# Kernel tuning notes

Hardware: AMD Instinct MI355X
Metric: run time of the kernel (lower is better)

Reference implementation:

```python
import jax, jax.numpy as jnp
import numpy as np

N, E, IN, OUT, R, B = 50000, 800000, 16, 16, 90, 30


def setup_inputs() -> dict:
    key = jax.random.key(0)
    ks = jax.random.split(key, 9)
    h = jax.random.normal(ks[0], (N, IN), dtype=jnp.float32)
    he = jax.random.normal(ks[1], (E, IN), dtype=jnp.float32)
    Ws = jax.random.normal(ks[2], (OUT, IN), dtype=jnp.float32) * 0.1      # shared_weight.weight
    Wa = jax.random.normal(ks[3], (1, 3 * OUT), dtype=jnp.float32) * 0.1   # attn_fc.weight
    weight = jax.random.normal(ks[4], (B, IN, OUT), dtype=jnp.float32) * 0.1  # basis weights
    w_comp = jax.random.normal(ks[5], (R, B), dtype=jnp.float32) * 0.1        # basis coefficients
    src = jax.random.randint(ks[6], (E,), 0, N)
    dst = jax.random.randint(ks[7], (E,), 0, N)
    rel_type = jax.random.randint(ks[8], (E,), 0, R)
    return {"h": h, "he": he, "Ws": Ws, "Wa": Wa, "weight": weight,
            "w_comp": w_comp, "src": src, "dst": dst, "rel_type": rel_type}


def reference(h, he, Ws, Wa, weight, w_comp, src, dst, rel_type):
    n_nodes, in_dim = h.shape
    num_bases, _, out_dim = weight.shape
    num_rels = w_comp.shape[0]

    # Basis decomposition, replicating the original's reshape semantics exactly:
    # view [B,in,out] -> [in,B,out], matmul with w_comp [R,B] -> [in,R,out], view -> [R,in,out]
    V = weight.reshape(in_dim, num_bases, out_dim)
    W_rel = jnp.matmul(w_comp, V).reshape(num_rels, in_dim, out_dim)  # [R,in,out]

    # edge_attention: GAT-like score from concat(z_src, z_edge, z_dst)
    h_src = h[src]                      # [E,in]
    z_src = h_src @ Ws.T                # [E,out]
    z_dst = h[dst] @ Ws.T               # [E,out]
    z_e = he @ Ws.T                     # [E,out]
    e = jnp.concatenate([z_src, z_e, z_dst], axis=1) @ Wa.T  # [E,1] (no leaky_relu / no softmax in original)

    # message: per-edge relation-specific bmm, scaled by attention score
    msg = jnp.einsum('ei,eio->eo', h_src, W_rel[rel_type]) * e  # [E,out]

    # reduce: scatter-sum into destination nodes (bias=None, activation=None)
    h_out = jax.ops.segment_sum(msg, dst, num_segments=n_nodes)  # [N,out]
    return h_out
```

## Files before the change

kernel.cpp:

```cpp
#include <hip/hip_runtime.h>

#define N_NODES 50000
#define N_EDGES 800000
#define IN_DIM 16
#define OUT_DIM 16
#define N_RELS 90
#define N_BASES 30

#define CAP 64
#define LDS_STRIDE 260

#define PREP_BLOCKS 91
#define DOTS_BLOCKS 196
#define ZERO_BLOCKS 196
#define HZ_BLOCKS 782

#define ROUTE_BLOCKS 3125
#define RNODES_PER_BLK 64
#define REDUCE_BLOCKS 782

__device__ __forceinline__ float4 shfl_xor4(float4 v, int m) {
    float4 r;
    r.x = __shfl_xor(v.x, m); r.y = __shfl_xor(v.y, m);
    r.z = __shfl_xor(v.z, m); r.w = __shfl_xor(v.w, m);
    return r;
}

__global__ __launch_bounds__(256) void setup_kernel(
    const float* __restrict__ Ws,
    const float* __restrict__ Wa,
    const float* __restrict__ weight,
    const float* __restrict__ w_comp,
    const float* __restrict__ h,
    float* __restrict__ Wrel,
    float* __restrict__ avec,
    float2* __restrict__ s13,
    int* __restrict__ cnt,
    float* __restrict__ hout)
{
    int b = blockIdx.x;
    if (b < PREP_BLOCKS) {
        int f = b * 256 + threadIdx.x;
        if (f < N_RELS * IN_DIM * OUT_DIM) {
            int a   = f / (N_RELS * OUT_DIM);
            int rem = f % (N_RELS * OUT_DIM);
            int r   = rem / OUT_DIM;
            int o   = rem % OUT_DIM;
            float acc = 0.f;
            #pragma unroll
            for (int bb = 0; bb < N_BASES; ++bb)
                acc += w_comp[r * N_BASES + bb] * weight[a * (N_BASES * OUT_DIM) + bb * OUT_DIM + o];
            Wrel[f] = acc;
        } else if (f < N_RELS * IN_DIM * OUT_DIM + 48) {
            int g = f - N_RELS * IN_DIM * OUT_DIM;
            int k = g / IN_DIM;
            int i = g % IN_DIM;
            float acc = 0.f;
            #pragma unroll
            for (int o = 0; o < OUT_DIM; ++o)
                acc += Wa[k * OUT_DIM + o] * Ws[o * IN_DIM + i];
            avec[g] = acc;
        }
    } else if (b < PREP_BLOCKS + DOTS_BLOCKS) {
        __shared__ float la[48];
        if (threadIdx.x < 48) {
            int k = threadIdx.x / IN_DIM;
            int i = threadIdx.x % IN_DIM;
            float acc = 0.f;
            #pragma unroll
            for (int o = 0; o < OUT_DIM; ++o)
                acc += Wa[k * OUT_DIM + o] * Ws[o * IN_DIM + i];
            la[threadIdx.x] = acc;
        }
        __syncthreads();
        int n = (b - PREP_BLOCKS) * 256 + threadIdx.x;
        if (n >= N_NODES) return;
        const float4* p = (const float4*)(h + (size_t)n * IN_DIM);
        float d1 = 0.f, d3 = 0.f;
        #pragma unroll
        for (int i = 0; i < 4; ++i) {
            float4 v = p[i];
            d1 += v.x * la[4*i+0] + v.y * la[4*i+1] + v.z * la[4*i+2] + v.w * la[4*i+3];
            d3 += v.x * la[32+4*i+0] + v.y * la[32+4*i+1] + v.z * la[32+4*i+2] + v.w * la[32+4*i+3];
        }
        s13[n] = make_float2(d1, d3);
    } else if (b < PREP_BLOCKS + DOTS_BLOCKS + ZERO_BLOCKS) {
        int n = (b - PREP_BLOCKS - DOTS_BLOCKS) * 256 + threadIdx.x;
        if (n < N_NODES) cnt[n] = 0;
    } else {
        int idx = (b - PREP_BLOCKS - DOTS_BLOCKS - ZERO_BLOCKS) * 256 + threadIdx.x;
        if (idx < N_NODES * OUT_DIM / 4) {
            float4 z = {0.f, 0.f, 0.f, 0.f};
            ((float4*)hout)[idx] = z;
        }
    }
}

__global__ __launch_bounds__(256) void route_kernel(
    const float* __restrict__ h,
    const float* __restrict__ he,
    const int* __restrict__ src,
    const int* __restrict__ dst,
    const int* __restrict__ rel,
    const float* __restrict__ Wrel,
    const float* __restrict__ avec,
    const float2* __restrict__ s13,
    int* __restrict__ cnt,
    uint2* __restrict__ bucket,
    float* __restrict__ hout)
{
    int e = blockIdx.x * 256 + threadIdx.x;
    if (e >= N_EDGES) return;
    int s = src[e], d = dst[e], r = rel[e];

    const float4* hep = (const float4*)(he + (size_t)e * IN_DIM);
    const float4* ap  = (const float4*)(avec + 16);
    float pd = 0.f;
    #pragma unroll
    for (int i = 0; i < 4; ++i) {
        float4 v = hep[i];
        float4 a = ap[i];
        pd += v.x * a.x + v.y * a.y + v.z * a.z + v.w * a.w;
    }

    int slot = atomicAdd(&cnt[d], 1);
    if (slot < CAP) {
        uint2 ent;
        ent.x = ((unsigned)r << 16) | (unsigned)s;
        ent.y = __float_as_uint(pd);
        bucket[(size_t)d * CAP + slot] = ent;
    } else {
        float2 ss = s13[s];
        float2 sd = s13[d];
        float score = ss.x + sd.y + pd;
        float hs[16];
        const float4* hp = (const float4*)(h + (size_t)s * IN_DIM);
        #pragma unroll
        for (int i = 0; i < 4; ++i) {
            float4 v = hp[i];
            hs[4*i+0] = v.x; hs[4*i+1] = v.y; hs[4*i+2] = v.z; hs[4*i+3] = v.w;
        }
        const float* W = Wrel + (size_t)r * 256;
        float* outp = hout + (size_t)d * OUT_DIM;
        #pragma unroll
        for (int o = 0; o < OUT_DIM; ++o) {
            float acc = 0.f;
            #pragma unroll
            for (int i = 0; i < IN_DIM; ++i) acc += hs[i] * W[i * OUT_DIM + o];
            atomicAdd(outp + o, acc * score);
        }
    }
}

__global__ __launch_bounds__(1024) void reduce_bmm_kernel(
    const float* __restrict__ h,
    const float* __restrict__ Wrel,
    const float2* __restrict__ s13,
    const uint2* __restrict__ bucket,
    const int* __restrict__ cnt,
    float* __restrict__ hout)
{
    extern __shared__ float lw[];
    for (int j = threadIdx.x; j < N_RELS * 64; j += 1024) {
        int r = j >> 6;
        int w = j & 63;
        float4 v = ((const float4*)Wrel)[r * 64 + w];
        *(float4*)(lw + r * LDS_STRIDE + w * 4) = v;
    }
    __syncthreads();

    int n = blockIdx.x * RNODES_PER_BLK + (threadIdx.x >> 4);
    int l = threadIdx.x & 15;
    int q = l & 3;
    int p = l >> 2;
    if (n >= N_NODES) return;

    int deg = cnt[n];
    int m = deg > CAP ? CAP : deg;
    const uint2* ep = bucket + (size_t)n * CAP;
    float s3n = s13[n].y;
    float4 acc = {0.f, 0.f, 0.f, 0.f};

    for (int j0 = 0; j0 < m; j0 += 8) {
        uint2 ent[2];
        float4 hq[2];
        float s1v[2];
        bool val[2];

        #pragma unroll
        for (int k = 0; k < 2; ++k) {
            int j = j0 + p * 2 + k;
            val[k] = (j < m);
            ent[k] = ep[val[k] ? j : 0];
        }

        #pragma unroll
        for (int k = 0; k < 2; ++k) {
            int sidx = ent[k].x & 0xFFFF;
            hq[k]  = *(const float4*)(h + (size_t)sidx * IN_DIM + q * 4);
            s1v[k] = s13[sidx].x;
        }

        #pragma unroll
        for (int k = 0; k < 2; ++k) {
            if (!val[k]) continue;
            int r = ent[k].x >> 16;
            float score = s1v[k] + s3n + __uint_as_float(ent[k].y);

            float4 o1 = shfl_xor4(hq[k], 1);
            float4 o2 = shfl_xor4(hq[k], 2);
            float4 o3 = shfl_xor4(o1, 2);
            bool q0 = (q == 0), q1 = (q == 1), q2 = (q == 2);
            float4 row0 = q0 ? hq[k] : q1 ? o1 : q2 ? o2 : o3;
            float4 row1 = q0 ? o1 : q1 ? hq[k] : q2 ? o3 : o2;
            float4 row2 = q0 ? o2 : q1 ? o3 : q2 ? hq[k] : o1;
            float4 row3 = q0 ? o3 : q1 ? o2 : q2 ? o1 : hq[k];
            float hs[16] = {row0.x,row0.y,row0.z,row0.w, row1.x,row1.y,row1.z,row1.w,
                            row2.x,row2.y,row2.z,row2.w, row3.x,row3.y,row3.z,row3.w};

            const float* wb = lw + (size_t)r * LDS_STRIDE + q * 4;
            float4 a = {0.f, 0.f, 0.f, 0.f};
            #pragma unroll
            for (int i = 0; i < 16; ++i) {
                float4 w = *(const float4*)(wb + i * 16);
                float hv = hs[i];
                a.x += hv * w.x; a.y += hv * w.y; a.z += hv * w.z; a.w += hv * w.w;
            }
            acc.x += score * a.x; acc.y += score * a.y;
            acc.z += score * a.z; acc.w += score * a.w;
        }
    }

    acc.x += __shfl_xor(acc.x, 4); acc.y += __shfl_xor(acc.y, 4);
    acc.z += __shfl_xor(acc.z, 4); acc.w += __shfl_xor(acc.w, 4);
    acc.x += __shfl_xor(acc.x, 8); acc.y += __shfl_xor(acc.y, 8);
    acc.z += __shfl_xor(acc.z, 8); acc.w += __shfl_xor(acc.w, 8);

    if (p == 0) {
        float* outp = hout + (size_t)n * OUT_DIM + q * 4;
        if (deg <= CAP) {
            *(float4*)outp = acc;
        } else {
            atomicAdd(outp + 0, acc.x);
            atomicAdd(outp + 1, acc.y);
            atomicAdd(outp + 2, acc.z);
            atomicAdd(outp + 3, acc.w);
        }
    }
}

__global__ __launch_bounds__(256) void prep_kernel(
    const float* __restrict__ Ws, const float* __restrict__ Wa,
    const float* __restrict__ weight, const float* __restrict__ w_comp,
    float* __restrict__ Wrel, float* __restrict__ avec)
{
    int f = blockIdx.x * blockDim.x + threadIdx.x;
    if (f < N_RELS * IN_DIM * OUT_DIM) {
        int a   = f / (N_RELS * OUT_DIM);
        int rem = f % (N_RELS * OUT_DIM);
        int r   = rem / OUT_DIM;
        int o   = rem % OUT_DIM;
        float acc = 0.f;
        #pragma unroll
        for (int b = 0; b < N_BASES; ++b)
            acc += w_comp[r * N_BASES + b] * weight[a * (N_BASES * OUT_DIM) + b * OUT_DIM + o];
        Wrel[f] = acc;
    } else if (f < N_RELS * IN_DIM * OUT_DIM + 48) {
        int g = f - N_RELS * IN_DIM * OUT_DIM;
        int k = g / IN_DIM;
        int i = g % IN_DIM;
        float acc = 0.f;
        #pragma unroll
        for (int o = 0; o < OUT_DIM; ++o)
            acc += Wa[k * OUT_DIM + o] * Ws[o * IN_DIM + i];
        avec[g] = acc;
    }
}

__global__ __launch_bounds__(256) void edge_atomic_kernel(
    const float* __restrict__ h,
    const float* __restrict__ he,
    const int* __restrict__ src,
    const int* __restrict__ dst,
    const int* __restrict__ rel,
    const float* __restrict__ Wrel,
    const float* __restrict__ avec,
    float* __restrict__ hout)
{
    int e = blockIdx.x * blockDim.x + threadIdx.x;
    if (e >= N_EDGES) return;
    int s = src[e], d = dst[e], r = rel[e];
    float hs[IN_DIM];
    const float4* p = (const float4*)(h + (size_t)s * IN_DIM);
    #pragma unroll
    for (int i = 0; i < 4; ++i) {
        float4 v = p[i];
        hs[4*i+0] = v.x; hs[4*i+1] = v.y; hs[4*i+2] = v.z; hs[4*i+3] = v.w;
    }
    float score = 0.f;
    #pragma unroll
    for (int i = 0; i < IN_DIM; ++i) score += hs[i] * avec[i];
    const float4* qe = (const float4*)(he + (size_t)e * IN_DIM);
    #pragma unroll
    for (int i = 0; i < 4; ++i) {
        float4 v = qe[i];
        score += v.x * avec[16+4*i] + v.y * avec[17+4*i] + v.z * avec[18+4*i] + v.w * avec[19+4*i];
    }
    const float4* pd = (const float4*)(h + (size_t)d * IN_DIM);
    #pragma unroll
    for (int i = 0; i < 4; ++i) {
        float4 v = pd[i];
        score += v.x * avec[32+4*i] + v.y * avec[33+4*i] + v.z * avec[34+4*i] + v.w * avec[35+4*i];
    }
    float acc[OUT_DIM];
    #pragma unroll
    for (int o = 0; o < OUT_DIM; ++o) acc[o] = 0.f;
    const float* W = Wrel + (size_t)r * 256;
    #pragma unroll
    for (int i = 0; i < IN_DIM; ++i) {
        float hv = hs[i];
        #pragma unroll
        for (int o = 0; o < OUT_DIM; ++o) acc[o] += hv * W[i * OUT_DIM + o];
    }
    float* outp = hout + (size_t)d * OUT_DIM;
    #pragma unroll
    for (int o = 0; o < OUT_DIM; ++o) atomicAdd(outp + o, acc[o] * score);
}

extern "C" void kernel_launch(void* const* d_in, const int* in_sizes, int n_in,
                              void* d_out, int out_size, void* d_ws, size_t ws_size,
                              hipStream_t stream) {
    const float* h      = (const float*)d_in[0];
    const float* he     = (const float*)d_in[1];
    const float* Ws     = (const float*)d_in[2];
    const float* Wa     = (const float*)d_in[3];
    const float* weight = (const float*)d_in[4];
    const float* w_comp = (const float*)d_in[5];
    const int*   src    = (const int*)d_in[6];
    const int*   dst    = (const int*)d_in[7];
    const int*   rel    = (const int*)d_in[8];
    float* hout = (float*)d_out;

    const size_t OFF_WREL   = 0;
    const size_t OFF_AVEC   = 23040;
    const size_t OFF_S13    = 23104;
    const size_t OFF_CNT    = 123104;
    const size_t OFF_BUCKET = 173104;
    const size_t NEED_BUCKET = OFF_BUCKET * 4 + (size_t)N_NODES * CAP * sizeof(uint2);

    float* wsf  = (float*)d_ws;
    float* Wrel = wsf + OFF_WREL;
    float* avec = wsf + OFF_AVEC;
    float2* s13 = (float2*)(wsf + OFF_S13);
    int* cnt    = (int*)(wsf + OFF_CNT);

    if (ws_size >= NEED_BUCKET) {
        uint2* bucket = (uint2*)(wsf + OFF_BUCKET);

        setup_kernel<<<PREP_BLOCKS + DOTS_BLOCKS + ZERO_BLOCKS + HZ_BLOCKS, 256, 0, stream>>>(
            Ws, Wa, weight, w_comp, h, Wrel, avec, s13, cnt, hout);
        route_kernel<<<ROUTE_BLOCKS, 256, 0, stream>>>(
            h, he, src, dst, rel, Wrel, avec, s13, cnt, bucket, hout);
        reduce_bmm_kernel<<<REDUCE_BLOCKS, 1024,
                            N_RELS * LDS_STRIDE * sizeof(float), stream>>>(
            h, Wrel, s13, bucket, cnt, hout);
    } else {
        hipMemsetAsync(d_out, 0, (size_t)out_size * sizeof(float), stream);
        int total = N_RELS * IN_DIM * OUT_DIM + 48;
        prep_kernel<<<(total + 255) / 256, 256, 0, stream>>>(Ws, Wa, weight, w_comp, Wrel, avec);
        edge_atomic_kernel<<<(N_EDGES + 255) / 256, 256, 0, stream>>>(
            h, he, src, dst, rel, Wrel, avec, hout);
    }
}
```

Baseline: 193.3 us.

## Persistent reduce blocks, wider edge batches, and shuffle-rotated bmm

The reduce kernel now launches 256 persistent blocks that grid-stride over nodes, so the 90-relation weight table is staged into LDS far fewer times. Each lane group handles 16 edges per iteration instead of 8, giving more loads in flight. The h row is pre-scaled by the score and combined with weights through xor-shuffle rotations instead of select chains. The float2 s13 array is split into separate s1 and s3 arrays, so gathers fetch only the needed scalar. Fewer blocks reduce parallelism and latency hiding for the gather-bound work, and larger batches raise register pressure.

```diff
diff --git a/kernel.cpp b/kernel.cpp
--- a/kernel.cpp
+++ b/kernel.cpp
@@ -16,8 +16,7 @@
 #define HZ_BLOCKS 782
 
 #define ROUTE_BLOCKS 3125
-#define RNODES_PER_BLK 64
-#define REDUCE_BLOCKS 782
+#define REDUCE_BLOCKS 256
 
 __device__ __forceinline__ float4 shfl_xor4(float4 v, int m) {
     float4 r;
@@ -34,7 +33,8 @@
     const float* __restrict__ h,
     float* __restrict__ Wrel,
     float* __restrict__ avec,
-    float2* __restrict__ s13,
+    float* __restrict__ s1,
+    float* __restrict__ s3,
     int* __restrict__ cnt,
     float* __restrict__ hout)
 {
@@ -83,7 +83,8 @@
             d1 += v.x * la[4*i+0] + v.y * la[4*i+1] + v.z * la[4*i+2] + v.w * la[4*i+3];
             d3 += v.x * la[32+4*i+0] + v.y * la[32+4*i+1] + v.z * la[32+4*i+2] + v.w * la[32+4*i+3];
         }
-        s13[n] = make_float2(d1, d3);
+        s1[n] = d1;
+        s3[n] = d3;
     } else if (b < PREP_BLOCKS + DOTS_BLOCKS + ZERO_BLOCKS) {
         int n = (b - PREP_BLOCKS - DOTS_BLOCKS) * 256 + threadIdx.x;
         if (n < N_NODES) cnt[n] = 0;
@@ -104,7 +105,8 @@
     const int* __restrict__ rel,
     const float* __restrict__ Wrel,
     const float* __restrict__ avec,
-    const float2* __restrict__ s13,
+    const float* __restrict__ s1,
+    const float* __restrict__ s3,
     int* __restrict__ cnt,
     uint2* __restrict__ bucket,
     float* __restrict__ hout)
@@ -130,9 +132,7 @@
         ent.y = __float_as_uint(pd);
         bucket[(size_t)d * CAP + slot] = ent;
     } else {
-        float2 ss = s13[s];
-        float2 sd = s13[d];
-        float score = ss.x + sd.y + pd;
+        float score = s1[s] + s3[d] + pd;
         float hs[16];
         const float4* hp = (const float4*)(h + (size_t)s * IN_DIM);
         #pragma unroll
@@ -155,7 +155,8 @@
 __global__ __launch_bounds__(1024) void reduce_bmm_kernel(
     const float* __restrict__ h,
     const float* __restrict__ Wrel,
-    const float2* __restrict__ s13,
+    const float* __restrict__ s1,
+    const float* __restrict__ s3,
     const uint2* __restrict__ bucket,
     const int* __restrict__ cnt,
     float* __restrict__ hout)
@@ -169,82 +170,78 @@
     }
     __syncthreads();
 
-    int n = blockIdx.x * RNODES_PER_BLK + (threadIdx.x >> 4);
-    int l = threadIdx.x & 15;
-    int q = l & 3;
-    int p = l >> 2;
-    if (n >= N_NODES) return;
-
-    int deg = cnt[n];
-    int m = deg > CAP ? CAP : deg;
-    const uint2* ep = bucket + (size_t)n * CAP;
-    float s3n = s13[n].y;
-    float4 acc = {0.f, 0.f, 0.f, 0.f};
-
-    for (int j0 = 0; j0 < m; j0 += 8) {
-        uint2 ent[2];
-        float4 hq[2];
-        float s1v[2];
-        bool val[2];
-
-        #pragma unroll
-        for (int k = 0; k < 2; ++k) {
-            int j = j0 + p * 2 + k;
-            val[k] = (j < m);
-            ent[k] = ep[val[k] ? j : 0];
-        }
-
-        #pragma unroll
-        for (int k = 0; k < 2; ++k) {
-            int sidx = ent[k].x & 0xFFFF;
-            hq[k]  = *(const float4*)(h + (size_t)sidx * IN_DIM + q * 4);
-            s1v[k] = s13[sidx].x;
-        }
-
-        #pragma unroll
-        for (int k = 0; k < 2; ++k) {
-            if (!val[k]) continue;
-            int r = ent[k].x >> 16;
-            float score = s1v[k] + s3n + __uint_as_float(ent[k].y);
-
-            float4 o1 = shfl_xor4(hq[k], 1);
-            float4 o2 = shfl_xor4(hq[k], 2);
-            float4 o3 = shfl_xor4(o1, 2);
-            bool q0 = (q == 0), q1 = (q == 1), q2 = (q == 2);
-            float4 row0 = q0 ? hq[k] : q1 ? o1 : q2 ? o2 : o3;
-            float4 row1 = q0 ? o1 : q1 ? hq[k] : q2 ? o3 : o2;
-            float4 row2 = q0 ? o2 : q1 ? o3 : q2 ? hq[k] : o1;
-            float4 row3 = q0 ? o3 : q1 ? o2 : q2 ? o1 : hq[k];
-            float hs[16] = {row0.x,row0.y,row0.z,row0.w, row1.x,row1.y,row1.z,row1.w,
-                            row2.x,row2.y,row2.z,row2.w, row3.x,row3.y,row3.z,row3.w};
-
-            const float* wb = lw + (size_t)r * LDS_STRIDE + q * 4;
-            float4 a = {0.f, 0.f, 0.f, 0.f};
-            #pragma unroll
-            for (int i = 0; i < 16; ++i) {
-                float4 w = *(const float4*)(wb + i * 16);
-                float hv = hs[i];
-                a.x += hv * w.x; a.y += hv * w.y; a.z += hv * w.z; a.w += hv * w.w;
+    const int l = threadIdx.x & 15;
+    const int q = l & 3;
+    const int p = l >> 2;
+    const int gsub = threadIdx.x >> 4;
+
+    for (int n = blockIdx.x * 64 + gsub; n < N_NODES; n += REDUCE_BLOCKS * 64) {
+        int deg = cnt[n];
+        int m = deg > CAP ? CAP : deg;
+        const uint2* ep = bucket + (size_t)n * CAP;
+        float s3n = s3[n];
+        float4 acc = {0.f, 0.f, 0.f, 0.f};
+
+        for (int j0 = 0; j0 < m; j0 += 16) {
+            uint2 ent[4];
+            float4 hq[4];
+            float s1v[4];
+            bool val[4];
+
+            #pragma unroll
+            for (int k = 0; k < 4; ++k) {
+                int j = j0 + p * 4 + k;
+                val[k] = (j < m);
+                ent[k] = ep[val[k] ? j : 0];
             }
-            acc.x += score * a.x; acc.y += score * a.y;
-            acc.z += score * a.z; acc.w += score * a.w;
-        }
-    }
-
-    acc.x += __shfl_xor(acc.x, 4); acc.y += __shfl_xor(acc.y, 4);
-    acc.z += __shfl_xor(acc.z, 4); acc.w += __shfl_xor(acc.w, 4);
-    acc.x += __shfl_xor(acc.x, 8); acc.y += __shfl_xor(acc.y, 8);
-    acc.z += __shfl_xor(acc.z, 8); acc.w += __shfl_xor(acc.w, 8);
-
-    if (p == 0) {
-        float* outp = hout + (size_t)n * OUT_DIM + q * 4;
-        if (deg <= CAP) {
-            *(float4*)outp = acc;
-        } else {
-            atomicAdd(outp + 0, acc.x);
-            atomicAdd(outp + 1, acc.y);
-            atomicAdd(outp + 2, acc.z);
-            atomicAdd(outp + 3, acc.w);
+
+            #pragma unroll
+            for (int k = 0; k < 4; ++k) {
+                int sidx = ent[k].x & 0xFFFF;
+                hq[k]  = *(const float4*)(h + (size_t)sidx * IN_DIM + q * 4);
+                s1v[k] = s1[sidx];
+            }
+
+            #pragma unroll
+            for (int k = 0; k < 4; ++k) {
+                if (!val[k]) continue;
+                unsigned rr = ent[k].x >> 16;
+                float score = s1v[k] + s3n + __uint_as_float(ent[k].y);
+                float4 hx = hq[k];
+                hx.x *= score; hx.y *= score; hx.z *= score; hx.w *= score;
+
+                const float* wb = lw + (size_t)rr * LDS_STRIDE + q * 4;
+                #pragma unroll
+                for (int mm = 0; mm < 4; ++mm) {
+                    float4 vm = (mm == 0) ? hx : shfl_xor4(hx, mm);
+                    const float* wrow = wb + (((unsigned)(q ^ mm)) << 6);
+                    float4 w0 = *(const float4*)(wrow +  0);
+                    float4 w1 = *(const float4*)(wrow + 16);
+                    float4 w2 = *(const float4*)(wrow + 32);
+                    float4 w3 = *(const float4*)(wrow + 48);
+                    acc.x += vm.x*w0.x + vm.y*w1.x + vm.z*w2.x + vm.w*w3.x;
+                    acc.y += vm.x*w0.y + vm.y*w1.y + vm.z*w2.y + vm.w*w3.y;
+                    acc.z += vm.x*w0.z + vm.y*w1.z + vm.z*w2.z + vm.w*w3.z;
+                    acc.w += vm.x*w0.w + vm.y*w1.w + vm.z*w2.w + vm.w*w3.w;
+                }
+            }
+        }
+
+        acc.x += __shfl_xor(acc.x, 4); acc.y += __shfl_xor(acc.y, 4);
+        acc.z += __shfl_xor(acc.z, 4); acc.w += __shfl_xor(acc.w, 4);
+        acc.x += __shfl_xor(acc.x, 8); acc.y += __shfl_xor(acc.y, 8);
+        acc.z += __shfl_xor(acc.z, 8); acc.w += __shfl_xor(acc.w, 8);
+
+        if (p == 0) {
+            float* outp = hout + (size_t)n * OUT_DIM + q * 4;
+            if (deg <= CAP) {
+                *(float4*)outp = acc;
+            } else {
+                atomicAdd(outp + 0, acc.x);
+                atomicAdd(outp + 1, acc.y);
+                atomicAdd(outp + 2, acc.z);
+                atomicAdd(outp + 3, acc.w);
+            }
         }
     }
 }
@@ -343,7 +340,8 @@
 
     const size_t OFF_WREL   = 0;
     const size_t OFF_AVEC   = 23040;
-    const size_t OFF_S13    = 23104;
+    const size_t OFF_S1     = 23104;
+    const size_t OFF_S3     = 73104;
     const size_t OFF_CNT    = 123104;
     const size_t OFF_BUCKET = 173104;
     const size_t NEED_BUCKET = OFF_BUCKET * 4 + (size_t)N_NODES * CAP * sizeof(uint2);
@@ -351,19 +349,20 @@
     float* wsf  = (float*)d_ws;
     float* Wrel = wsf + OFF_WREL;
     float* avec = wsf + OFF_AVEC;
-    float2* s13 = (float2*)(wsf + OFF_S13);
+    float* s1   = wsf + OFF_S1;
+    float* s3   = wsf + OFF_S3;
     int* cnt    = (int*)(wsf + OFF_CNT);
 
     if (ws_size >= NEED_BUCKET) {
         uint2* bucket = (uint2*)(wsf + OFF_BUCKET);
 
         setup_kernel<<<PREP_BLOCKS + DOTS_BLOCKS + ZERO_BLOCKS + HZ_BLOCKS, 256, 0, stream>>>(
-            Ws, Wa, weight, w_comp, h, Wrel, avec, s13, cnt, hout);
+            Ws, Wa, weight, w_comp, h, Wrel, avec, s1, s3, cnt, hout);
         route_kernel<<<ROUTE_BLOCKS, 256, 0, stream>>>(
-            h, he, src, dst, rel, Wrel, avec, s13, cnt, bucket, hout);
+            h, he, src, dst, rel, Wrel, avec, s1, s3, cnt, bucket, hout);
         reduce_bmm_kernel<<<REDUCE_BLOCKS, 1024,
                             N_RELS * LDS_STRIDE * sizeof(float), stream>>>(
-            h, Wrel, s13, bucket, cnt, hout);
+            h, Wrel, s1, s3, bucket, cnt, hout);
     } else {
         hipMemsetAsync(d_out, 0, (size_t)out_size * sizeof(float), stream);
         int total = N_RELS * IN_DIM * OUT_DIM + 48;
```

Result: no change. 190.3 us (-1.6%).
